# Kernel optimization log

Hardware: AMD Instinct MI355X
Metric: run time of the kernel (lower is better)

## Reference

```python
import jax, jax.numpy as jnp
import numpy as np

EMBED_DIM = 1024
NUM_HEADS = 16
HEAD_DIM = EMBED_DIM // NUM_HEADS
SCALE = HEAD_DIM ** -0.5


def setup_inputs() -> dict:
    key = jax.random.key(0)
    k1, k2, k3, k4 = jax.random.split(key, 4)
    B, N, D = 2, 2048, EMBED_DIM
    x = jax.random.normal(k1, (B, N, D), dtype=jnp.float32)
    # nn.Linear weights stored as [out, in]; we keep [in, out] for x @ W
    w_qkv = jax.random.normal(k2, (D, 3 * D), dtype=jnp.float32) * (D ** -0.5)
    w_proj = jax.random.normal(k3, (D, D), dtype=jnp.float32) * (D ** -0.5)
    b_proj = jax.random.normal(k4, (D,), dtype=jnp.float32) * 0.01
    return {"x": x, "w_qkv": w_qkv, "w_proj": w_proj, "b_proj": b_proj}


def reference(x, w_qkv, w_proj, b_proj):
    B, N, D = x.shape
    H, Hd = NUM_HEADS, HEAD_DIM
    qkv = x @ w_qkv  # [B, N, 3D]
    q, k, v = jnp.split(qkv, 3, axis=-1)
    # [B, N, D] -> [B, H, N, Hd]
    split_heads = lambda t: t.reshape(B, N, H, Hd).transpose(0, 2, 1, 3)
    q, k, v = split_heads(q), split_heads(k), split_heads(v)
    a = jnp.einsum("bhqd,bhkd->bhqk", q, k) * SCALE
    a = jax.nn.softmax(a, axis=-1)
    out = jnp.einsum("bhqk,bhkd->bhqd", a, v)
    out = out.transpose(0, 2, 1, 3).reshape(B, N, D)
    return out @ w_proj + b_proj
```

## Files before the change

### kernel.cpp

```cpp
#include <hip/hip_runtime.h>
#include <stdint.h>

typedef __attribute__((ext_vector_type(8))) short bf16x8;
typedef __attribute__((ext_vector_type(4))) float f32x4;
typedef __attribute__((ext_vector_type(4))) float float4v;
typedef __attribute__((ext_vector_type(8))) unsigned short u16x8;

#define DEV __device__ __forceinline__

DEV unsigned short f2bf(float f) {
    union { float f; uint32_t u; } v; v.f = f;
    uint32_t u = v.u;
    return (unsigned short)((u + 0x7FFFu + ((u >> 16) & 1u)) >> 16);
}

DEV unsigned int cvt_pk_bf16(float lo, float hi) {
    unsigned int r;
    asm("v_cvt_pk_bf16_f32 %0, %1, %2" : "=v"(r) : "v"(lo), "v"(hi));
    return r;
}

#if __has_builtin(__builtin_amdgcn_global_load_lds)
#define HAVE_GLDS 1
typedef const unsigned char __attribute__((address_space(1)))* as1p;
typedef unsigned char __attribute__((address_space(3)))* as3p;
DEV void gload16(const unsigned short* g, unsigned short* l) {
    __builtin_amdgcn_global_load_lds((as1p)(const void*)g, (as3p)(void*)l, 16, 0, 0);
}
#else
#define HAVE_GLDS 0
#endif

__global__ void k_cvt_x(const float* __restrict__ x, unsigned short* __restrict__ xb, int n4) {
    int i = blockIdx.x * blockDim.x + threadIdx.x;
    if (i >= n4) return;
    float4v v = *(const float4v*)(x + (size_t)i * 4);
    union { unsigned short s[4]; uint64_t q; } o;
    o.s[0] = f2bf(v[0]); o.s[1] = f2bf(v[1]); o.s[2] = f2bf(v[2]); o.s[3] = f2bf(v[3]);
    *(uint64_t*)(xb + (size_t)i * 4) = o.q;
}

__global__ void k_cvt_tr_w(const float* __restrict__ w, unsigned short* __restrict__ wt,
                           int R, int C) {
    __shared__ alignas(16) unsigned short tile[64][65];
    const int t = threadIdx.x;
    const int tr = blockIdx.y * 64, tc = blockIdx.x * 64;
#pragma unroll
    for (int p = 0; p < 4; ++p) {
        int r = p * 16 + (t >> 4);
        int c = (t & 15) * 4;
        float4v v = *(const float4v*)(w + (size_t)(tr + r) * C + tc + c);
#pragma unroll
        for (int j = 0; j < 4; ++j) tile[r][c + j] = f2bf(v[j]);
    }
    __syncthreads();
#pragma unroll
    for (int p = 0; p < 2; ++p) {
        int r2 = p * 32 + (t >> 3);
        int k0 = (t & 7) * 8;
        u16x8 o;
#pragma unroll
        for (int j = 0; j < 8; ++j) o[j] = tile[k0 + j][r2];
        *(u16x8*)(wt + (size_t)(tc + r2) * R + tr + k0) = o;
    }
}

template <int OUT_BF16, int BN>
__global__ __launch_bounds__(256)
void k_gemm_bt(const unsigned short* __restrict__ A,
               const unsigned short* __restrict__ Bt,
               void* __restrict__ Cp, const float* __restrict__ bias,
               unsigned short* __restrict__ vt_out,
               int M, int N, int K) {
    constexpr int NFR = BN / 32;
    __shared__ alignas(16) unsigned short lA[128 * 64];
    __shared__ alignas(16) unsigned short lB[BN * 64];
    const int t = threadIdx.x;
    const int w = t >> 6, l = t & 63;
    const int l15 = l & 15, l4 = l >> 4;
    const int wm = (w >> 1) * 64, wn = (w & 1) * (BN / 2);
    const size_t bm = (size_t)blockIdx.y * 128, bn = (size_t)blockIdx.x * BN;

    int offA[4][2], offB[NFR][2];
#pragma unroll
    for (int f = 0; f < 4; ++f) {
        const int ra = wm + f * 16 + l15;
#pragma unroll
        for (int kc = 0; kc < 2; ++kc)
            offA[f][kc] = ra * 64 + (((kc * 4 + l4) ^ (ra & 7)) << 3);
    }
#pragma unroll
    for (int f = 0; f < NFR; ++f) {
        const int rb = wn + f * 16 + l15;
#pragma unroll
        for (int kc = 0; kc < 2; ++kc)
            offB[f][kc] = rb * 64 + (((kc * 4 + l4) ^ (rb & 7)) << 3);
    }

#if HAVE_GLDS
    const int srow8 = l >> 3;
    const int scol  = (l & 7) ^ srow8;
    const unsigned short* gA = A  + (bm + w * 32 + srow8) * (size_t)K + scol * 8;
    const unsigned short* gB = Bt + (bn + w * (BN / 4) + srow8) * (size_t)K + scol * 8;
    unsigned short* dA = lA + (w * 32) * 64;
    unsigned short* dB = lB + (w * (BN / 4)) * 64;
#else
    const int srow = t >> 3, sslot = t & 7;
    const int swoff = srow * 64 + ((sslot ^ (srow & 7)) << 3);
    const unsigned short* pA = A + (bm + srow) * (size_t)K + sslot * 8;
    const unsigned short* pB = Bt + (bn + srow) * (size_t)K + sslot * 8;
#endif

    const f32x4 zf = {0.f, 0.f, 0.f, 0.f};
    f32x4 acc[4][NFR];
#pragma unroll
    for (int i = 0; i < 4; ++i)
#pragma unroll
        for (int j = 0; j < NFR; ++j) acc[i][j] = zf;

    for (int kt = 0; kt < K; kt += 64) {
#if HAVE_GLDS
        __syncthreads();
#pragma unroll
        for (int i = 0; i < 4; ++i)
            gload16(gA + (size_t)i * 8 * K + kt, dA + i * 8 * 64);
#pragma unroll
        for (int i = 0; i < BN / 32; ++i)
            gload16(gB + (size_t)i * 8 * K + kt, dB + i * 8 * 64);
        __syncthreads();
#else
        bf16x8 ra[4], rb[BN / 32];
#pragma unroll
        for (int p = 0; p < 4; ++p)
            ra[p] = *(const bf16x8*)(pA + (size_t)p * 32 * K + kt);
#pragma unroll
        for (int p = 0; p < BN / 32; ++p)
            rb[p] = *(const bf16x8*)(pB + (size_t)p * 32 * K + kt);
        __syncthreads();
#pragma unroll
        for (int p = 0; p < 4; ++p)
            *(bf16x8*)(lA + p * 32 * 64 + swoff) = ra[p];
#pragma unroll
        for (int p = 0; p < BN / 32; ++p)
            *(bf16x8*)(lB + p * 32 * 64 + swoff) = rb[p];
        __syncthreads();
#endif
#pragma unroll
        for (int kc = 0; kc < 2; ++kc) {
            bf16x8 af[4], bfr[NFR];
#pragma unroll
            for (int f = 0; f < 4; ++f) af[f] = *(const bf16x8*)(lA + offA[f][kc]);
#pragma unroll
            for (int f = 0; f < NFR; ++f) bfr[f] = *(const bf16x8*)(lB + offB[f][kc]);
#pragma unroll
            for (int mf = 0; mf < 4; ++mf)
#pragma unroll
                for (int nf = 0; nf < NFR; ++nf)
                    acc[mf][nf] = __builtin_amdgcn_mfma_f32_16x16x32_bf16(
                        af[mf], bfr[nf], acc[mf][nf], 0, 0, 0);
        }
    }

    if (OUT_BF16) {
        if (vt_out && bn >= 2048) {
            const int bb = (int)(bm >> 11);
            const int n0 = (int)(bm & 2047) + wm + l4 * 4;
#pragma unroll
            for (int nf = 0; nf < NFR; ++nf) {
                const int d = (int)(bn - 2048) + wn + nf * 16 + l15;
                unsigned short* vrow = vt_out + ((size_t)(bb * 16 + (d >> 6)) * 64 + (d & 63)) * 2048;
#pragma unroll
                for (int mf = 0; mf < 4; ++mf) {
                    union { unsigned short s[4]; uint64_t q; } u;
#pragma unroll
                    for (int j = 0; j < 4; ++j) u.s[j] = f2bf(acc[mf][nf][j]);
                    *(uint64_t*)(vrow + n0 + mf * 16) = u.q;
                }
            }
        } else {
            unsigned short* C = (unsigned short*)Cp;
#pragma unroll
            for (int mf = 0; mf < 4; ++mf)
#pragma unroll
                for (int nf = 0; nf < NFR; ++nf) {
                    const size_t row = bm + wm + mf * 16 + l4 * 4;
                    const size_t col = bn + wn + nf * 16 + l15;
#pragma unroll
                    for (int j = 0; j < 4; ++j)
                        C[(row + j) * (size_t)N + col] = f2bf(acc[mf][nf][j]);
                }
        }
    } else {
        float* C = (float*)Cp;
#pragma unroll
        for (int nf = 0; nf < NFR; ++nf) {
            const size_t col = bn + wn + nf * 16 + l15;
            const float bv = bias[col];
#pragma unroll
            for (int mf = 0; mf < 4; ++mf) {
                const size_t row = bm + wm + mf * 16 + l4 * 4;
#pragma unroll
                for (int j = 0; j < 4; ++j)
                    C[(row + j) * (size_t)N + col] = acc[mf][nf][j] + bv;
            }
        }
    }
}

__global__ __launch_bounds__(256, 4)
void k_attn(const unsigned short* __restrict__ qkv, const unsigned short* __restrict__ vt,
            unsigned short* __restrict__ attn_out) {
    __shared__ alignas(16) unsigned short lK[2][64 * 64];
    __shared__ alignas(16) unsigned short lV[2][64 * 64];
    __shared__ alignas(16) unsigned short lP[4][16 * 64];
    const int t = threadIdx.x, w = t >> 6, l = t & 63;
    const int l15 = l & 15, l4 = l >> 4;
    const int bh = blockIdx.y, b = bh >> 4, h = bh & 15;
    const int qb = blockIdx.x * 64;
    const float QSCALE = 0.18033688011112042f;

    const unsigned short* qptr =
        qkv + (size_t)(b * 2048 + qb + w * 16 + l15) * 3072 + h * 64 + l4 * 8;
    const bf16x8 aq0 = *(const bf16x8*)(qptr);
    const bf16x8 aq1 = *(const bf16x8*)(qptr + 32);

    const int srow = t >> 3, sslot = t & 7;
    const int swoff = srow * 64 + ((sslot ^ (srow & 7)) << 3);
    const unsigned short* kptr = qkv + (size_t)(b * 2048 + srow) * 3072 + 1024 + h * 64 + sslot * 8;
    const unsigned short* vptr = vt + (size_t)(bh * 64 + srow) * 2048 + sslot * 8;

    int offK[4][2];
#pragma unroll
    for (int nf = 0; nf < 4; ++nf) {
        const int r = nf * 16 + l15;
#pragma unroll
        for (int kc = 0; kc < 2; ++kc)
            offK[nf][kc] = r * 64 + (((kc * 4 + l4) ^ (r & 7)) << 3);
    }
    int offPw[4];
#pragma unroll
    for (int nf = 0; nf < 4; ++nf) {
        const int c = nf * 16 + l4 * 4;
        offPw[nf] = l15 * 64 + (((c >> 3) ^ (l15 & 7)) << 3) + (c & 7);
    }

    const f32x4 zf = {0.f, 0.f, 0.f, 0.f};
    f32x4 o[4];
#pragma unroll
    for (int df = 0; df < 4; ++df) o[df] = zf;
    f32x4 accl = zf;
    float m_run = -1e30f;
    unsigned short* Pw = &lP[w][0];
    const bf16x8 ones8 = {(short)0x3F80, (short)0x3F80, (short)0x3F80, (short)0x3F80,
                          (short)0x3F80, (short)0x3F80, (short)0x3F80, (short)0x3F80};

    {
        bf16x8 rk[2], rv[2];
#pragma unroll
        for (int p = 0; p < 2; ++p) {
            rk[p] = *(const bf16x8*)(kptr + (size_t)(p * 32) * 3072);
            rv[p] = *(const bf16x8*)(vptr + (size_t)(p * 32) * 2048);
        }
#pragma unroll
        for (int p = 0; p < 2; ++p) {
            *(bf16x8*)(&lK[0][0] + p * 32 * 64 + swoff) = rk[p];
            *(bf16x8*)(&lV[0][0] + p * 32 * 64 + swoff) = rv[p];
        }
        __syncthreads();
    }

#pragma unroll 2
    for (int kt = 0; kt < 2048; kt += 64) {
        const int cur = (kt >> 6) & 1;
        const unsigned short* K = &lK[cur][0];
        const unsigned short* V = &lV[cur][0];

        bf16x8 rk[2], rv[2];
        const bool more = (kt + 64) < 2048;
        if (more) {
#pragma unroll
            for (int p = 0; p < 2; ++p) {
                rk[p] = *(const bf16x8*)(kptr + (size_t)(kt + 64 + p * 32) * 3072);
                rv[p] = *(const bf16x8*)(vptr + (size_t)(p * 32) * 2048 + kt + 64);
            }
        }

        f32x4 s[4];
        __builtin_amdgcn_s_setprio(1);
#pragma unroll
        for (int nf = 0; nf < 4; ++nf) {
            const bf16x8 kf0 = *(const bf16x8*)(K + offK[nf][0]);
            const bf16x8 kf1 = *(const bf16x8*)(K + offK[nf][1]);
            f32x4 a = zf;
            a = __builtin_amdgcn_mfma_f32_16x16x32_bf16(kf0, aq0, a, 0, 0, 0);
            a = __builtin_amdgcn_mfma_f32_16x16x32_bf16(kf1, aq1, a, 0, 0, 0);
            s[nf] = a;
        }
        __builtin_amdgcn_s_setprio(0);

        float mx = fmaxf(fmaxf(s[0][0], s[0][1]), s[0][2]);
        mx = fmaxf(fmaxf(mx, s[0][3]), s[1][0]);
        mx = fmaxf(fmaxf(mx, s[1][1]), s[1][2]);
        mx = fmaxf(fmaxf(mx, s[1][3]), s[2][0]);
        mx = fmaxf(fmaxf(mx, s[2][1]), s[2][2]);
        mx = fmaxf(fmaxf(mx, s[2][3]), s[3][0]);
        mx = fmaxf(fmaxf(mx, s[3][1]), s[3][2]);
        mx = fmaxf(mx, s[3][3]);
        mx = fmaxf(mx, __shfl_xor(mx, 16));
        mx = fmaxf(mx, __shfl_xor(mx, 32));
        mx *= QSCALE;

        if (!__all(mx <= m_run + 8.0f)) {
            const float mn = fmaxf(m_run, mx);
            const float alpha = exp2f(m_run - mn);
            m_run = mn;
            const float a0 = __shfl(alpha, l4 * 4 + 0);
            const float a1 = __shfl(alpha, l4 * 4 + 1);
            const float a2 = __shfl(alpha, l4 * 4 + 2);
            const float a3 = __shfl(alpha, l4 * 4 + 3);
#pragma unroll
            for (int df = 0; df < 4; ++df) {
                o[df][0] *= a0; o[df][1] *= a1; o[df][2] *= a2; o[df][3] *= a3;
            }
            accl[0] *= a0; accl[1] *= a1; accl[2] *= a2; accl[3] *= a3;
        }

#pragma unroll
        for (int nf = 0; nf < 4; ++nf) {
            const float p0 = exp2f(fmaf(s[nf][0], QSCALE, -m_run));
            const float p1 = exp2f(fmaf(s[nf][1], QSCALE, -m_run));
            const float p2 = exp2f(fmaf(s[nf][2], QSCALE, -m_run));
            const float p3 = exp2f(fmaf(s[nf][3], QSCALE, -m_run));
            union { unsigned int d[2]; uint64_t q; } u;
            u.d[0] = cvt_pk_bf16(p0, p1);
            u.d[1] = cvt_pk_bf16(p2, p3);
            *(uint64_t*)(Pw + offPw[nf]) = u.q;
        }

        const bf16x8 ap0 = *(const bf16x8*)(Pw + l15 * 64 + ((l4 ^ (l15 & 7)) << 3));
        const bf16x8 ap1 = *(const bf16x8*)(Pw + l15 * 64 + (((4 + l4) ^ (l15 & 7)) << 3));
        __builtin_amdgcn_s_setprio(1);
        accl = __builtin_amdgcn_mfma_f32_16x16x32_bf16(ap0, ones8, accl, 0, 0, 0);
        accl = __builtin_amdgcn_mfma_f32_16x16x32_bf16(ap1, ones8, accl, 0, 0, 0);
#pragma unroll
        for (int df = 0; df < 4; ++df) {
            const int r = df * 16 + l15;
            const bf16x8 bv0 = *(const bf16x8*)(V + r * 64 + ((l4 ^ (r & 7)) << 3));
            const bf16x8 bv1 = *(const bf16x8*)(V + r * 64 + (((4 + l4) ^ (r & 7)) << 3));
            o[df] = __builtin_amdgcn_mfma_f32_16x16x32_bf16(ap0, bv0, o[df], 0, 0, 0);
            o[df] = __builtin_amdgcn_mfma_f32_16x16x32_bf16(ap1, bv1, o[df], 0, 0, 0);
        }
        __builtin_amdgcn_s_setprio(0);

        if (more) {
#pragma unroll
            for (int p = 0; p < 2; ++p) {
                *(bf16x8*)(&lK[cur ^ 1][0] + p * 32 * 64 + swoff) = rk[p];
                *(bf16x8*)(&lV[cur ^ 1][0] + p * 32 * 64 + swoff) = rv[p];
            }
        }
        __syncthreads();
    }

    const float r0 = 1.0f / accl[0];
    const float r1 = 1.0f / accl[1];
    const float r2 = 1.0f / accl[2];
    const float r3 = 1.0f / accl[3];
    const int rowb = b * 2048 + qb + w * 16 + l4 * 4;
#pragma unroll
    for (int df = 0; df < 4; ++df) {
        const int d = df * 16 + l15;
        attn_out[(size_t)(rowb + 0) * 1024 + h * 64 + d] = f2bf(o[df][0] * r0);
        attn_out[(size_t)(rowb + 1) * 1024 + h * 64 + d] = f2bf(o[df][1] * r1);
        attn_out[(size_t)(rowb + 2) * 1024 + h * 64 + d] = f2bf(o[df][2] * r2);
        attn_out[(size_t)(rowb + 3) * 1024 + h * 64 + d] = f2bf(o[df][3] * r3);
    }
}

extern "C" void kernel_launch(void* const* d_in, const int* in_sizes, int n_in,
                              void* d_out, int out_size, void* d_ws, size_t ws_size,
                              hipStream_t stream) {
    const float* x      = (const float*)d_in[0];
    const float* w_qkv  = (const float*)d_in[1];
    const float* w_proj = (const float*)d_in[2];
    const float* b_proj = (const float*)d_in[3];
    float* out = (float*)d_out;

    char* ws = (char*)d_ws;
    unsigned short* xb     = (unsigned short*)(ws + 0);
    unsigned short* wqkvT  = (unsigned short*)(ws + 8388608);
    unsigned short* wprojT = (unsigned short*)(ws + 14680064);
    unsigned short* qkv    = (unsigned short*)(ws + 16777216);
    unsigned short* vt     = (unsigned short*)(ws + 41943040);
    unsigned short* attn   = (unsigned short*)(ws + 50331648);

    k_cvt_x<<<dim3(4096), dim3(256), 0, stream>>>(x, xb, 4096 * 1024 / 4);
    k_cvt_tr_w<<<dim3(48, 16), dim3(256), 0, stream>>>(w_qkv, wqkvT, 1024, 3072);
    k_cvt_tr_w<<<dim3(16, 16), dim3(256), 0, stream>>>(w_proj, wprojT, 1024, 1024);
    k_gemm_bt<1, 128><<<dim3(24, 32), dim3(256), 0, stream>>>(xb, wqkvT, (void*)qkv, (const float*)nullptr, vt, 4096, 3072, 1024);
    k_attn<<<dim3(32, 32), dim3(256), 0, stream>>>(qkv, vt, attn);
    k_gemm_bt<0, 64><<<dim3(16, 32), dim3(256), 0, stream>>>(attn, wprojT, (void*)out, b_proj, (unsigned short*)nullptr, 4096, 1024, 1024);
}
```

Measured before the change: 133.2 us.

## Process two query sub-tiles per wave in attention to reuse K/V tiles

```diff
diff --git a/kernel.cpp b/kernel.cpp
--- a/kernel.cpp
+++ b/kernel.cpp
@@ -207,22 +207,26 @@
     }
 }
 
-__global__ __launch_bounds__(256, 4)
+__global__ __launch_bounds__(256, 2)
 void k_attn(const unsigned short* __restrict__ qkv, const unsigned short* __restrict__ vt,
             unsigned short* __restrict__ attn_out) {
     __shared__ alignas(16) unsigned short lK[2][64 * 64];
     __shared__ alignas(16) unsigned short lV[2][64 * 64];
-    __shared__ alignas(16) unsigned short lP[4][16 * 64];
+    __shared__ alignas(16) unsigned short lP[4][2][16 * 64];
     const int t = threadIdx.x, w = t >> 6, l = t & 63;
     const int l15 = l & 15, l4 = l >> 4;
     const int bh = blockIdx.y, b = bh >> 4, h = bh & 15;
-    const int qb = blockIdx.x * 64;
+    const int qb = blockIdx.x * 128;
     const float QSCALE = 0.18033688011112042f;
 
-    const unsigned short* qptr =
-        qkv + (size_t)(b * 2048 + qb + w * 16 + l15) * 3072 + h * 64 + l4 * 8;
-    const bf16x8 aq0 = *(const bf16x8*)(qptr);
-    const bf16x8 aq1 = *(const bf16x8*)(qptr + 32);
+    bf16x8 aq[2][2];
+#pragma unroll
+    for (int qs = 0; qs < 2; ++qs) {
+        const unsigned short* qptr =
+            qkv + (size_t)(b * 2048 + qb + w * 32 + qs * 16 + l15) * 3072 + h * 64 + l4 * 8;
+        aq[qs][0] = *(const bf16x8*)(qptr);
+        aq[qs][1] = *(const bf16x8*)(qptr + 32);
+    }
 
     const int srow = t >> 3, sslot = t & 7;
     const int swoff = srow * 64 + ((sslot ^ (srow & 7)) << 3);
@@ -245,12 +249,13 @@
     }
 
     const f32x4 zf = {0.f, 0.f, 0.f, 0.f};
-    f32x4 o[4];
-#pragma unroll
-    for (int df = 0; df < 4; ++df) o[df] = zf;
-    f32x4 accl = zf;
-    float m_run = -1e30f;
-    unsigned short* Pw = &lP[w][0];
+    f32x4 o[2][4];
+#pragma unroll
+    for (int qs = 0; qs < 2; ++qs)
+#pragma unroll
+        for (int df = 0; df < 4; ++df) o[qs][df] = zf;
+    f32x4 accl[2] = {zf, zf};
+    float m_run[2] = {-1e30f, -1e30f};
     const bf16x8 ones8 = {(short)0x3F80, (short)0x3F80, (short)0x3F80, (short)0x3F80,
                           (short)0x3F80, (short)0x3F80, (short)0x3F80, (short)0x3F80};
 
@@ -269,7 +274,6 @@
         __syncthreads();
     }
 
-#pragma unroll 2
     for (int kt = 0; kt < 2048; kt += 64) {
         const int cur = (kt >> 6) & 1;
         const unsigned short* K = &lK[cur][0];
@@ -285,70 +289,101 @@
             }
         }
 
-        f32x4 s[4];
+        bf16x8 kf[4][2];
+#pragma unroll
+        for (int nf = 0; nf < 4; ++nf) {
+            kf[nf][0] = *(const bf16x8*)(K + offK[nf][0]);
+            kf[nf][1] = *(const bf16x8*)(K + offK[nf][1]);
+        }
+
+        f32x4 s[2][4];
         __builtin_amdgcn_s_setprio(1);
 #pragma unroll
-        for (int nf = 0; nf < 4; ++nf) {
-            const bf16x8 kf0 = *(const bf16x8*)(K + offK[nf][0]);
-            const bf16x8 kf1 = *(const bf16x8*)(K + offK[nf][1]);
-            f32x4 a = zf;
-            a = __builtin_amdgcn_mfma_f32_16x16x32_bf16(kf0, aq0, a, 0, 0, 0);
-            a = __builtin_amdgcn_mfma_f32_16x16x32_bf16(kf1, aq1, a, 0, 0, 0);
-            s[nf] = a;
-        }
+        for (int qs = 0; qs < 2; ++qs)
+#pragma unroll
+            for (int nf = 0; nf < 4; ++nf) {
+                f32x4 a = zf;
+                a = __builtin_amdgcn_mfma_f32_16x16x32_bf16(kf[nf][0], aq[qs][0], a, 0, 0, 0);
+                a = __builtin_amdgcn_mfma_f32_16x16x32_bf16(kf[nf][1], aq[qs][1], a, 0, 0, 0);
+                s[qs][nf] = a;
+            }
         __builtin_amdgcn_s_setprio(0);
 
-        float mx = fmaxf(fmaxf(s[0][0], s[0][1]), s[0][2]);
-        mx = fmaxf(fmaxf(mx, s[0][3]), s[1][0]);
-        mx = fmaxf(fmaxf(mx, s[1][1]), s[1][2]);
-        mx = fmaxf(fmaxf(mx, s[1][3]), s[2][0]);
-        mx = fmaxf(fmaxf(mx, s[2][1]), s[2][2]);
-        mx = fmaxf(fmaxf(mx, s[2][3]), s[3][0]);
-        mx = fmaxf(fmaxf(mx, s[3][1]), s[3][2]);
-        mx = fmaxf(mx, s[3][3]);
-        mx = fmaxf(mx, __shfl_xor(mx, 16));
-        mx = fmaxf(mx, __shfl_xor(mx, 32));
-        mx *= QSCALE;
-
-        if (!__all(mx <= m_run + 8.0f)) {
-            const float mn = fmaxf(m_run, mx);
-            const float alpha = exp2f(m_run - mn);
-            m_run = mn;
-            const float a0 = __shfl(alpha, l4 * 4 + 0);
-            const float a1 = __shfl(alpha, l4 * 4 + 1);
-            const float a2 = __shfl(alpha, l4 * 4 + 2);
-            const float a3 = __shfl(alpha, l4 * 4 + 3);
-#pragma unroll
-            for (int df = 0; df < 4; ++df) {
-                o[df][0] *= a0; o[df][1] *= a1; o[df][2] *= a2; o[df][3] *= a3;
-            }
-            accl[0] *= a0; accl[1] *= a1; accl[2] *= a2; accl[3] *= a3;
-        }
-
-#pragma unroll
-        for (int nf = 0; nf < 4; ++nf) {
-            const float p0 = exp2f(fmaf(s[nf][0], QSCALE, -m_run));
-            const float p1 = exp2f(fmaf(s[nf][1], QSCALE, -m_run));
-            const float p2 = exp2f(fmaf(s[nf][2], QSCALE, -m_run));
-            const float p3 = exp2f(fmaf(s[nf][3], QSCALE, -m_run));
-            union { unsigned int d[2]; uint64_t q; } u;
-            u.d[0] = cvt_pk_bf16(p0, p1);
-            u.d[1] = cvt_pk_bf16(p2, p3);
-            *(uint64_t*)(Pw + offPw[nf]) = u.q;
-        }
-
-        const bf16x8 ap0 = *(const bf16x8*)(Pw + l15 * 64 + ((l4 ^ (l15 & 7)) << 3));
-        const bf16x8 ap1 = *(const bf16x8*)(Pw + l15 * 64 + (((4 + l4) ^ (l15 & 7)) << 3));
+        float mx[2];
+#pragma unroll
+        for (int qs = 0; qs < 2; ++qs) {
+            float m = fmaxf(fmaxf(s[qs][0][0], s[qs][0][1]), s[qs][0][2]);
+            m = fmaxf(fmaxf(m, s[qs][0][3]), s[qs][1][0]);
+            m = fmaxf(fmaxf(m, s[qs][1][1]), s[qs][1][2]);
+            m = fmaxf(fmaxf(m, s[qs][1][3]), s[qs][2][0]);
+            m = fmaxf(fmaxf(m, s[qs][2][1]), s[qs][2][2]);
+            m = fmaxf(fmaxf(m, s[qs][2][3]), s[qs][3][0]);
+            m = fmaxf(fmaxf(m, s[qs][3][1]), s[qs][3][2]);
+            m = fmaxf(m, s[qs][3][3]);
+            m = fmaxf(m, __shfl_xor(m, 16));
+            m = fmaxf(m, __shfl_xor(m, 32));
+            mx[qs] = m * QSCALE;
+        }
+
+        if (!__all(mx[0] <= m_run[0] + 8.0f && mx[1] <= m_run[1] + 8.0f)) {
+#pragma unroll
+            for (int qs = 0; qs < 2; ++qs) {
+                const float mn = fmaxf(m_run[qs], mx[qs]);
+                const float alpha = exp2f(m_run[qs] - mn);
+                m_run[qs] = mn;
+                const float a0 = __shfl(alpha, l4 * 4 + 0);
+                const float a1 = __shfl(alpha, l4 * 4 + 1);
+                const float a2 = __shfl(alpha, l4 * 4 + 2);
+                const float a3 = __shfl(alpha, l4 * 4 + 3);
+#pragma unroll
+                for (int df = 0; df < 4; ++df) {
+                    o[qs][df][0] *= a0; o[qs][df][1] *= a1;
+                    o[qs][df][2] *= a2; o[qs][df][3] *= a3;
+                }
+                accl[qs][0] *= a0; accl[qs][1] *= a1;
+                accl[qs][2] *= a2; accl[qs][3] *= a3;
+            }
+        }
+
+#pragma unroll
+        for (int qs = 0; qs < 2; ++qs) {
+            unsigned short* Pw = &lP[w][qs][0];
+#pragma unroll
+            for (int nf = 0; nf < 4; ++nf) {
+                const float p0 = exp2f(fmaf(s[qs][nf][0], QSCALE, -m_run[qs]));
+                const float p1 = exp2f(fmaf(s[qs][nf][1], QSCALE, -m_run[qs]));
+                const float p2 = exp2f(fmaf(s[qs][nf][2], QSCALE, -m_run[qs]));
+                const float p3 = exp2f(fmaf(s[qs][nf][3], QSCALE, -m_run[qs]));
+                union { unsigned int d[2]; uint64_t q; } u;
+                u.d[0] = cvt_pk_bf16(p0, p1);
+                u.d[1] = cvt_pk_bf16(p2, p3);
+                *(uint64_t*)(Pw + offPw[nf]) = u.q;
+            }
+        }
+
+        bf16x8 ap[2][2];
+#pragma unroll
+        for (int qs = 0; qs < 2; ++qs) {
+            unsigned short* Pw = &lP[w][qs][0];
+            ap[qs][0] = *(const bf16x8*)(Pw + l15 * 64 + ((l4 ^ (l15 & 7)) << 3));
+            ap[qs][1] = *(const bf16x8*)(Pw + l15 * 64 + (((4 + l4) ^ (l15 & 7)) << 3));
+        }
         __builtin_amdgcn_s_setprio(1);
-        accl = __builtin_amdgcn_mfma_f32_16x16x32_bf16(ap0, ones8, accl, 0, 0, 0);
-        accl = __builtin_amdgcn_mfma_f32_16x16x32_bf16(ap1, ones8, accl, 0, 0, 0);
+#pragma unroll
+        for (int qs = 0; qs < 2; ++qs) {
+            accl[qs] = __builtin_amdgcn_mfma_f32_16x16x32_bf16(ap[qs][0], ones8, accl[qs], 0, 0, 0);
+            accl[qs] = __builtin_amdgcn_mfma_f32_16x16x32_bf16(ap[qs][1], ones8, accl[qs], 0, 0, 0);
+        }
 #pragma unroll
         for (int df = 0; df < 4; ++df) {
             const int r = df * 16 + l15;
             const bf16x8 bv0 = *(const bf16x8*)(V + r * 64 + ((l4 ^ (r & 7)) << 3));
             const bf16x8 bv1 = *(const bf16x8*)(V + r * 64 + (((4 + l4) ^ (r & 7)) << 3));
-            o[df] = __builtin_amdgcn_mfma_f32_16x16x32_bf16(ap0, bv0, o[df], 0, 0, 0);
-            o[df] = __builtin_amdgcn_mfma_f32_16x16x32_bf16(ap1, bv1, o[df], 0, 0, 0);
+#pragma unroll
+            for (int qs = 0; qs < 2; ++qs) {
+                o[qs][df] = __builtin_amdgcn_mfma_f32_16x16x32_bf16(ap[qs][0], bv0, o[qs][df], 0, 0, 0);
+                o[qs][df] = __builtin_amdgcn_mfma_f32_16x16x32_bf16(ap[qs][1], bv1, o[qs][df], 0, 0, 0);
+            }
         }
         __builtin_amdgcn_s_setprio(0);
 
@@ -362,18 +397,21 @@
         __syncthreads();
     }
 
-    const float r0 = 1.0f / accl[0];
-    const float r1 = 1.0f / accl[1];
-    const float r2 = 1.0f / accl[2];
-    const float r3 = 1.0f / accl[3];
-    const int rowb = b * 2048 + qb + w * 16 + l4 * 4;
-#pragma unroll
-    for (int df = 0; df < 4; ++df) {
-        const int d = df * 16 + l15;
-        attn_out[(size_t)(rowb + 0) * 1024 + h * 64 + d] = f2bf(o[df][0] * r0);
-        attn_out[(size_t)(rowb + 1) * 1024 + h * 64 + d] = f2bf(o[df][1] * r1);
-        attn_out[(size_t)(rowb + 2) * 1024 + h * 64 + d] = f2bf(o[df][2] * r2);
-        attn_out[(size_t)(rowb + 3) * 1024 + h * 64 + d] = f2bf(o[df][3] * r3);
+#pragma unroll
+    for (int qs = 0; qs < 2; ++qs) {
+        const float r0 = 1.0f / accl[qs][0];
+        const float r1 = 1.0f / accl[qs][1];
+        const float r2 = 1.0f / accl[qs][2];
+        const float r3 = 1.0f / accl[qs][3];
+        const int rowb = b * 2048 + qb + w * 32 + qs * 16 + l4 * 4;
+#pragma unroll
+        for (int df = 0; df < 4; ++df) {
+            const int d = df * 16 + l15;
+            attn_out[(size_t)(rowb + 0) * 1024 + h * 64 + d] = f2bf(o[qs][df][0] * r0);
+            attn_out[(size_t)(rowb + 1) * 1024 + h * 64 + d] = f2bf(o[qs][df][1] * r1);
+            attn_out[(size_t)(rowb + 2) * 1024 + h * 64 + d] = f2bf(o[qs][df][2] * r2);
+            attn_out[(size_t)(rowb + 3) * 1024 + h * 64 + d] = f2bf(o[qs][df][3] * r3);
+        }
     }
 }
 
@@ -398,6 +436,6 @@
     k_cvt_tr_w<<<dim3(48, 16), dim3(256), 0, stream>>>(w_qkv, wqkvT, 1024, 3072);
     k_cvt_tr_w<<<dim3(16, 16), dim3(256), 0, stream>>>(w_proj, wprojT, 1024, 1024);
     k_gemm_bt<1, 128><<<dim3(24, 32), dim3(256), 0, stream>>>(xb, wqkvT, (void*)qkv, (const float*)nullptr, vt, 4096, 3072, 1024);
-    k_attn<<<dim3(32, 32), dim3(256), 0, stream>>>(qkv, vt, attn);
+    k_attn<<<dim3(16, 32), dim3(256), 0, stream>>>(qkv, vt, attn);
     k_gemm_bt<0, 64><<<dim3(16, 32), dim3(256), 0, stream>>>(attn, wprojT, (void*)out, b_proj, (unsigned short*)nullptr, 4096, 1024, 1024);
 }
```

Measured after the change: 134.2 us. No clear change (+0.7%).
